# Kernel optimization log

Hardware: AMD Instinct MI355X
Metric: run time of the kernel (lower is better)

## Reference

```python
import jax, jax.numpy as jnp
import numpy as np

B, T, C, H = 4, 4096, 1024, 64  # batch, seq_len, embedding_dimension, head_size


def setup_inputs() -> dict:
    key = jax.random.key(0)
    kx, kq, kk, kv = jax.random.split(key, 4)
    x = jax.random.normal(kx, (B, T, C), dtype=jnp.float32)
    # nn.Linear(C, H, bias=False) -> weight applied as x @ W with W:[C,H]
    s = 1.0 / np.sqrt(C)
    Wq = jax.random.normal(kq, (C, H), dtype=jnp.float32) * s
    Wk = jax.random.normal(kk, (C, H), dtype=jnp.float32) * s
    Wv = jax.random.normal(kv, (C, H), dtype=jnp.float32) * s
    return {"x": x, "Wq": Wq, "Wk": Wk, "Wv": Wv}


def reference(x, Wq, Wk, Wv):
    Bx, Tx, Cx = x.shape
    q = x @ Wq  # [B,T,H]
    k = x @ Wk  # [B,T,H]
    v = x @ Wv  # [B,T,H]
    # NOTE: original scales by C**-0.5 (embedding dim), not head_size**-0.5
    wei = jnp.einsum('bqh,bkh->bqk', q, k) * (Cx ** -0.5)  # [B,T,T]
    causal = jnp.tril(jnp.ones((Tx, Tx), dtype=bool))
    wei = jnp.where(causal, wei, -jnp.inf)
    wei = jax.nn.softmax(wei, axis=-1)
    out = jnp.einsum('bqk,bkh->bqh', wei, v)  # [B,T,H]
    return out
```

## Files before the change

kernel.cpp:

```cpp
#include <hip/hip_runtime.h>
#include <math.h>

#define BATCH 4
#define SEQ   4096
#define EMB   1024
#define HDIM  64
#define NSPLIT 4

typedef __attribute__((ext_vector_type(8))) short bf16x8;
typedef __attribute__((ext_vector_type(4))) float f32x4;
typedef __attribute__((ext_vector_type(16))) float f32x16;
typedef __attribute__((ext_vector_type(4))) unsigned int u32x4;

#define MFMA16(a, b, c) __builtin_amdgcn_mfma_f32_16x16x32_bf16(a, b, c, 0, 0, 0)
#define MFMA32(a, b, c) __builtin_amdgcn_mfma_f32_32x32x16_bf16(a, b, c, 0, 0, 0)
#define ZERO16 (f32x16){0.f,0.f,0.f,0.f,0.f,0.f,0.f,0.f,0.f,0.f,0.f,0.f,0.f,0.f,0.f,0.f}

__device__ __forceinline__ unsigned short f2bf(float f) {
  unsigned int u = __float_as_uint(f);
  u = (u + 0x7FFFu + ((u >> 16) & 1u)) >> 16;
  return (unsigned short)u;
}

__device__ __forceinline__ float fexp2(float x) {
  float r;
  asm("v_exp_f32 %0, %1" : "=v"(r) : "v"(x));
  return r;
}

__global__ __launch_bounds__(256) void wt_kernel(
    const float* __restrict__ Wq, const float* __restrict__ Wk,
    const float* __restrict__ Wv, unsigned short* __restrict__ wt) {
  __shared__ float tile[64][65];
  const int bid = blockIdx.x;
  const int m = bid >> 4, kt = bid & 15;
  const float* W = (m == 0) ? Wq : (m == 1) ? Wk : Wv;
  const int tid = threadIdx.x;
  {
    const int r = tid >> 2, c4 = tid & 3;
    const float* src = W + (size_t)(kt * 64 + r) * 64 + c4 * 16;
#pragma unroll
    for (int j = 0; j < 4; ++j) {
      float4 a = *(const float4*)(src + j * 4);
      tile[r][c4 * 16 + j * 4 + 0] = a.x;
      tile[r][c4 * 16 + j * 4 + 1] = a.y;
      tile[r][c4 * 16 + j * 4 + 2] = a.z;
      tile[r][c4 * 16 + j * 4 + 3] = a.w;
    }
  }
  __syncthreads();
  {
    const int col = tid >> 2, kq = tid & 3;
    unsigned short o[16];
#pragma unroll
    for (int j = 0; j < 16; ++j) o[j] = f2bf(tile[kq * 16 + j][col]);
    unsigned short* dst = wt + (size_t)(m * 64 + col) * 1024 + kt * 64 + kq * 16;
    *(bf16x8*)(dst)     = *(bf16x8*)&o[0];
    *(bf16x8*)(dst + 8) = *(bf16x8*)&o[8];
  }
}

__global__ __launch_bounds__(512) void qkv_mfma_kernel(
    const float* __restrict__ x, const unsigned short* __restrict__ wt,
    unsigned short* __restrict__ qb, unsigned short* __restrict__ kb,
    unsigned short* __restrict__ vt) {
  __shared__ __align__(16) unsigned short xs[64 * 64];
  __shared__ __align__(16) unsigned short ws[192 * 64];
  const int tid  = threadIdx.x;
  const int lane = tid & 63, wid = tid >> 6;
  const int g = lane >> 4, p = lane & 15;
  const int mt = wid >> 2, wq = wid & 3;
  const size_t row0 = (size_t)blockIdx.x * 64;

  const int sr = tid >> 3, sc = tid & 7;
  const float* xp = x + (row0 + sr) * EMB + sc * 8;

  f32x4 acc[2][3];
#pragma unroll
  for (int rt = 0; rt < 2; ++rt)
#pragma unroll
    for (int ct = 0; ct < 3; ++ct) acc[rt][ct] = (f32x4){0.f, 0.f, 0.f, 0.f};

  float4 rx[2];
  bf16x8 rw[3];
#pragma unroll
  for (int j = 0; j < 2; ++j) rx[j] = *(const float4*)(xp + j * 4);
#pragma unroll
  for (int it = 0; it < 3; ++it) {
    int i = tid + it * 512, col = i >> 3, cc = i & 7;
    rw[it] = *(const bf16x8*)(wt + (size_t)col * 1024 + cc * 8);
  }

  for (int kc = 0; kc < 16; ++kc) {
    __syncthreads();
#pragma unroll
    for (int j = 0; j < 2; ++j) {
      ushort4 h;
      h.x = f2bf(rx[j].x); h.y = f2bf(rx[j].y);
      h.z = f2bf(rx[j].z); h.w = f2bf(rx[j].w);
      *(ushort4*)((char*)xs + ((sr * 128 + sc * 16 + j * 8) ^ ((sr & 7) << 4))) = h;
    }
#pragma unroll
    for (int it = 0; it < 3; ++it) {
      int i = tid + it * 512, col = i >> 3, cc = i & 7;
      *(bf16x8*)((char*)ws + ((col * 128 + cc * 16) ^ ((col & 7) << 4))) = rw[it];
    }
    if (kc < 15) {
      const float* xpn = xp + (kc + 1) * 64;
#pragma unroll
      for (int j = 0; j < 2; ++j) rx[j] = *(const float4*)(xpn + j * 4);
#pragma unroll
      for (int it = 0; it < 3; ++it) {
        int i = tid + it * 512, col = i >> 3, cc = i & 7;
        rw[it] = *(const bf16x8*)(wt + (size_t)col * 1024 + (kc + 1) * 64 + cc * 8);
      }
    }
    __syncthreads();
#pragma unroll
    for (int ks = 0; ks < 2; ++ks) {
      bf16x8 af[2];
#pragma unroll
      for (int rt = 0; rt < 2; ++rt) {
        int row = mt * 32 + rt * 16 + p;
        af[rt] = *(const bf16x8*)((char*)xs +
                 ((row * 128 + ks * 64 + g * 16) ^ ((row & 7) << 4)));
      }
#pragma unroll
      for (int ct = 0; ct < 3; ++ct) {
        int col = wq * 48 + ct * 16 + p;
        bf16x8 bfr = *(const bf16x8*)((char*)ws +
                     ((col * 128 + ks * 64 + g * 16) ^ ((col & 7) << 4)));
#pragma unroll
        for (int rt = 0; rt < 2; ++rt)
          acc[rt][ct] = MFMA16(af[rt], bfr, acc[rt][ct]);
      }
    }
  }

  const int b     = (int)(row0 >> 12);
  const int tbase = (int)(row0 & 4095);
  unsigned short* vtb = vt + (((size_t)b * 64 + (tbase >> 6)) * 64) * 64;
#pragma unroll
  for (int rt = 0; rt < 2; ++rt)
#pragma unroll
    for (int ct = 0; ct < 3; ++ct) {
      const int c0  = wq * 48 + ct * 16;
      const int mtx = c0 >> 6;
      const int col = (c0 & 63) + p;
#pragma unroll
      for (int r = 0; r < 4; ++r) {
        const int row = mt * 32 + rt * 16 + 4 * g + r;
        const float vf = acc[rt][ct][r];
        if (mtx == 0)      qb[(row0 + row) * HDIM + col] = f2bf(vf * 0.0450843714f);
        else if (mtx == 1) kb[(row0 + row) * HDIM + col] = f2bf(vf);
        else               vtb[(size_t)col * 64 + row]   = f2bf(vf);
      }
    }
}

__device__ __forceinline__ void tile_body32(
    const unsigned short* __restrict__ sKb, const unsigned short* __restrict__ sVb,
    int qrel, bool diag, const bf16x8 (&qf)[4], int h, int q5,
    float& m, float& l, f32x16& o0, f32x16& o1) {
  const int sw = (q5 & 7) << 4;
  f32x16 s0 = ZERO16, s1 = ZERO16;
#pragma unroll
  for (int st = 0; st < 4; ++st) {
    bf16x8 k0 = *(const bf16x8*)((const char*)sKb + q5 * 128 +
                                 ((32 * st + 16 * h) ^ sw));
    bf16x8 k1 = *(const bf16x8*)((const char*)sKb + (32 + q5) * 128 +
                                 ((32 * st + 16 * h) ^ sw));
    s0 = MFMA32(k0, qf[st], s0);
    s1 = MFMA32(k1, qf[st], s1);
  }
  if (diag) {
#pragma unroll
    for (int r = 0; r < 16; ++r) {
      const int kk = (r & 3) + 8 * (r >> 2) + 4 * h;
      if (kk      > qrel) s0[r] = -1e30f;
      if (kk + 32 > qrel) s1[r] = -1e30f;
    }
  }
  float tm = -3e38f;
#pragma unroll
  for (int r = 0; r < 16; ++r) { tm = fmaxf(tm, s0[r]); tm = fmaxf(tm, s1[r]); }
  tm = fmaxf(tm, __shfl_xor(tm, 32));
  if (__any(tm > m + 11.5f)) {
    float mn = fmaxf(m, tm);
    float c = fexp2(m - mn);
    l *= c; o0 *= c; o1 *= c;
    m = mn;
  }
  float ps = 0.f;
#pragma unroll
  for (int r = 0; r < 16; ++r) {
    float a = fexp2(s0[r] - m); s0[r] = a; ps += a;
    float c2 = fexp2(s1[r] - m); s1[r] = c2; ps += c2;
  }
  ps += __shfl_xor(ps, 32);
  l += ps;
  unsigned W[16];
#pragma unroll
  for (int i = 0; i < 8; ++i) {
    asm("v_cvt_pk_bf16_f32 %0, %1, %2" : "=v"(W[i])     : "v"(s0[2*i]), "v"(s0[2*i+1]));
    asm("v_cvt_pk_bf16_f32 %0, %1, %2" : "=v"(W[8 + i]) : "v"(s1[2*i]), "v"(s1[2*i+1]));
  }
  bf16x8 pf[4];
#pragma unroll
  for (int sG = 0; sG < 4; ++sG) {
    const int ba = 4 * sG;
    unsigned x0 = (unsigned)__shfl_xor((int)W[ba + 0], 32);
    unsigned x1 = (unsigned)__shfl_xor((int)W[ba + 1], 32);
    unsigned x2 = (unsigned)__shfl_xor((int)W[ba + 2], 32);
    unsigned x3 = (unsigned)__shfl_xor((int)W[ba + 3], 32);
    u32x4 fw;
    fw[0] = h ? x2 : W[ba + 0];
    fw[1] = h ? x3 : W[ba + 1];
    fw[2] = h ? W[ba + 2] : x0;
    fw[3] = h ? W[ba + 3] : x1;
    pf[sG] = __builtin_bit_cast(bf16x8, fw);
  }
#pragma unroll
  for (int sG = 0; sG < 4; ++sG) {
    bf16x8 v0 = *(const bf16x8*)((const char*)sVb + q5 * 128 +
                                 ((32 * sG + 16 * h) ^ sw));
    o0 = MFMA32(v0, pf[sG], o0);
    bf16x8 v1 = *(const bf16x8*)((const char*)sVb + (32 + q5) * 128 +
                                 ((32 * sG + 16 * h) ^ sw));
    o1 = MFMA32(v1, pf[sG], o1);
  }
}

__device__ __forceinline__ void item_map128(int g_it, int nA, int nB,
                                            int& kt, bool& isA, bool& diag) {
  if (g_it < nA) { isA = true;  kt = g_it;      diag = (kt >= nA - 2); }
  else           { isA = false; kt = g_it - nA; diag = (kt >= nB - 2); }
}

__global__ __launch_bounds__(512) void attn_partial_kernel(
    const unsigned short* __restrict__ qb, const unsigned short* __restrict__ kbm,
    const unsigned short* __restrict__ vt, float* __restrict__ pw) {
  __shared__ __align__(16) unsigned short sK[2][4096];
  __shared__ __align__(16) unsigned short sV[2][4096];
  const int tid = threadIdx.x;
  const int wid = tid >> 6, lane = tid & 63;
  const int q5 = lane & 31, h = lane >> 5;
  const int bid = blockIdx.x;
  const int sp = bid & 3, j = (bid >> 2) & 15, b = bid >> 6;
  const int jB = 31 - j;
  const int nA = 2 * j + 2, nB = 64 - 2 * j;
  const bool sideA = (wid < 4);
  const int ws = sideA ? wid : wid - 4;
  const int tq0 = sideA ? j * 128 + 32 * ws : jB * 128 + 32 * ws;

  const char* kbase = (const char*)(kbm + (size_t)b * SEQ * HDIM);
  const char* vbase = (const char*)(vt  + (size_t)b * SEQ * HDIM);

  bf16x8 qf[4];
  {
    const unsigned short* qrow = qb + ((size_t)b * SEQ + tq0 + q5) * HDIM;
#pragma unroll
    for (int st = 0; st < 4; ++st)
      qf[st] = *(const bf16x8*)(qrow + 16 * st + 8 * h);
  }

  const int slot = tid * 16;
  const int r0 = slot >> 7, koff = r0 * 128 + ((slot & 127) ^ ((r0 & 7) << 4));

  float m = -1e30f, l = 0.f;
  f32x16 o0 = ZERO16, o1 = ZERO16;

  const int cnt = (66 - sp + NSPLIT - 1) / NSPLIT;

  bf16x8 rk0, rv0;
  {
    int kt; bool isA, diag;
    item_map128(sp, nA, nB, kt, isA, diag);
    rk0 = *(const bf16x8*)(kbase + (size_t)kt * 8192 + koff);
    rv0 = *(const bf16x8*)(vbase + (size_t)kt * 8192 + koff);
  }
  *(bf16x8*)((char*)sK[0] + slot) = rk0;
  *(bf16x8*)((char*)sV[0] + slot) = rv0;
  if (cnt > 1) {
    int kt; bool isA, diag;
    item_map128(sp + NSPLIT, nA, nB, kt, isA, diag);
    rk0 = *(const bf16x8*)(kbase + (size_t)kt * 8192 + koff);
    rv0 = *(const bf16x8*)(vbase + (size_t)kt * 8192 + koff);
  }
  __syncthreads();

  for (int ii = 0; ii < cnt; ++ii) {
    const int buf = ii & 1;
    if (ii + 1 < cnt) {
      const int nb = buf ^ 1;
      *(bf16x8*)((char*)sK[nb] + slot) = rk0;
      *(bf16x8*)((char*)sV[nb] + slot) = rv0;
    }
    if (ii + 2 < cnt) {
      int kt; bool isA, diag;
      item_map128(sp + (ii + 2) * NSPLIT, nA, nB, kt, isA, diag);
      rk0 = *(const bf16x8*)(kbase + (size_t)kt * 8192 + koff);
      rv0 = *(const bf16x8*)(vbase + (size_t)kt * 8192 + koff);
    }
    int kt; bool isA, diag;
    item_map128(sp + ii * NSPLIT, nA, nB, kt, isA, diag);
    if (isA == sideA) {
      tile_body32(sK[buf], sV[buf], tq0 + q5 - kt * 64, diag, qf, h, q5,
                  m, l, o0, o1);
    }
    __syncthreads();
  }

  l += __shfl_xor(l, 32);
  l *= 0.5f;

  const int grp = (sideA ? j * 8 + 2 * ws : jB * 8 + 2 * ws) + (q5 >> 4);
  float* pp = pw + ((size_t)(b * 256 + grp) * NSPLIT + sp) * 1056;
  const int qr = (q5 & 15) * 64;
#pragma unroll
  for (int quad = 0; quad < 4; ++quad) {
    *(f32x4*)(pp + qr + 8 * quad + 4 * h) =
        (f32x4){o0[4 * quad], o0[4 * quad + 1], o0[4 * quad + 2], o0[4 * quad + 3]};
    *(f32x4*)(pp + qr + 32 + 8 * quad + 4 * h) =
        (f32x4){o1[4 * quad], o1[4 * quad + 1], o1[4 * quad + 2], o1[4 * quad + 3]};
  }
  if (h == 0) { pp[1024 + (q5 & 15)] = m; pp[1040 + (q5 & 15)] = l; }
}

__global__ __launch_bounds__(256) void attn_merge_kernel(
    const float* __restrict__ pw, float* __restrict__ out) {
  const int bid = blockIdx.x;
  const int b = bid >> 8, grp = bid & 255;
  const int q = threadIdx.x & 15, db = threadIdx.x >> 4;
  const float* pp = pw + (size_t)bid * NSPLIT * 1056;
  float ms[NSPLIT], ls[NSPLIT];
  float mm = -3e38f;
#pragma unroll
  for (int s = 0; s < NSPLIT; ++s) {
    ms[s] = pp[s * 1056 + 1024 + q];
    ls[s] = pp[s * 1056 + 1040 + q];
    mm = fmaxf(mm, ms[s]);
  }
  float L = 0.f, a0 = 0.f, a1 = 0.f, a2 = 0.f, a3 = 0.f;
#pragma unroll
  for (int s = 0; s < NSPLIT; ++s) {
    float sc = fexp2(ms[s] - mm);
    L += ls[s] * sc;
    float4 v = *(const float4*)(pp + s * 1056 + q * 64 + 4 * db);
    a0 += v.x * sc; a1 += v.y * sc; a2 += v.z * sc; a3 += v.w * sc;
  }
  const float inv = 1.f / L;
  float* op = out + ((size_t)b * SEQ + grp * 16 + q) * HDIM + 4 * db;
  op[0] = a0 * inv; op[1] = a1 * inv; op[2] = a2 * inv; op[3] = a3 * inv;
}

extern "C" void kernel_launch(void* const* d_in, const int* in_sizes, int n_in,
                              void* d_out, int out_size, void* d_ws, size_t ws_size,
                              hipStream_t stream) {
  const float* x  = (const float*)d_in[0];
  const float* Wq = (const float*)d_in[1];
  const float* Wk = (const float*)d_in[2];
  const float* Wv = (const float*)d_in[3];
  float* outp = (float*)d_out;

  const size_t rows = (size_t)BATCH * SEQ;
  unsigned short* qbf = (unsigned short*)d_ws;
  unsigned short* kbf = qbf + rows * HDIM;
  unsigned short* vtb = kbf + rows * HDIM;
  unsigned short* wt  = vtb + rows * HDIM;
  float* pw = (float*)(wt + 192 * 1024);

  wt_kernel<<<dim3(48), dim3(256), 0, stream>>>(Wq, Wk, Wv, wt);
  qkv_mfma_kernel<<<dim3((unsigned)(rows / 64)), dim3(512), 0, stream>>>(x, wt, qbf, kbf, vtb);
  attn_partial_kernel<<<dim3(256), dim3(512), 0, stream>>>(qbf, kbf, vtb, pw);
  attn_merge_kernel<<<dim3(1024), dim3(256), 0, stream>>>(pw, outp);
}
```

Baseline: 56.61 us.

## Process two KV tiles per step with both wave groups handling both query sides

```diff
diff --git a/kernel.cpp b/kernel.cpp
--- a/kernel.cpp
+++ b/kernel.cpp
@@ -240,91 +240,112 @@
 __global__ __launch_bounds__(512) void attn_partial_kernel(
     const unsigned short* __restrict__ qb, const unsigned short* __restrict__ kbm,
     const unsigned short* __restrict__ vt, float* __restrict__ pw) {
-  __shared__ __align__(16) unsigned short sK[2][4096];
-  __shared__ __align__(16) unsigned short sV[2][4096];
+  __shared__ __align__(16) unsigned short sK[4][4096];
+  __shared__ __align__(16) unsigned short sV[4][4096];
   const int tid = threadIdx.x;
   const int wid = tid >> 6, lane = tid & 63;
   const int q5 = lane & 31, h = lane >> 5;
+  const int gg = wid >> 2, ws = wid & 3;
   const int bid = blockIdx.x;
   const int sp = bid & 3, j = (bid >> 2) & 15, b = bid >> 6;
   const int jB = 31 - j;
   const int nA = 2 * j + 2, nB = 64 - 2 * j;
-  const bool sideA = (wid < 4);
-  const int ws = sideA ? wid : wid - 4;
-  const int tq0 = sideA ? j * 128 + 32 * ws : jB * 128 + 32 * ws;
+  const int tq0A = j * 128 + 32 * ws;
+  const int tq0B = jB * 128 + 32 * ws;
 
   const char* kbase = (const char*)(kbm + (size_t)b * SEQ * HDIM);
   const char* vbase = (const char*)(vt  + (size_t)b * SEQ * HDIM);
 
-  bf16x8 qf[4];
-  {
-    const unsigned short* qrow = qb + ((size_t)b * SEQ + tq0 + q5) * HDIM;
-#pragma unroll
-    for (int st = 0; st < 4; ++st)
-      qf[st] = *(const bf16x8*)(qrow + 16 * st + 8 * h);
+  bf16x8 qfA[4], qfB[4];
+  {
+    const unsigned short* qra = qb + ((size_t)b * SEQ + tq0A + q5) * HDIM;
+    const unsigned short* qrb = qb + ((size_t)b * SEQ + tq0B + q5) * HDIM;
+#pragma unroll
+    for (int st = 0; st < 4; ++st) {
+      qfA[st] = *(const bf16x8*)(qra + 16 * st + 8 * h);
+      qfB[st] = *(const bf16x8*)(qrb + 16 * st + 8 * h);
+    }
   }
 
   const int slot = tid * 16;
   const int r0 = slot >> 7, koff = r0 * 128 + ((slot & 127) ^ ((r0 & 7) << 4));
 
-  float m = -1e30f, l = 0.f;
-  f32x16 o0 = ZERO16, o1 = ZERO16;
+  float mA = -1e30f, lA = 0.f, mB = -1e30f, lB = 0.f;
+  f32x16 oA0 = ZERO16, oA1 = ZERO16, oB0 = ZERO16, oB1 = ZERO16;
 
   const int cnt = (66 - sp + NSPLIT - 1) / NSPLIT;
 
-  bf16x8 rk0, rv0;
-  {
-    int kt; bool isA, diag;
-    item_map128(sp, nA, nB, kt, isA, diag);
-    rk0 = *(const bf16x8*)(kbase + (size_t)kt * 8192 + koff);
-    rv0 = *(const bf16x8*)(vbase + (size_t)kt * 8192 + koff);
-  }
-  *(bf16x8*)((char*)sK[0] + slot) = rk0;
-  *(bf16x8*)((char*)sV[0] + slot) = rv0;
-  if (cnt > 1) {
-    int kt; bool isA, diag;
-    item_map128(sp + NSPLIT, nA, nB, kt, isA, diag);
-    rk0 = *(const bf16x8*)(kbase + (size_t)kt * 8192 + koff);
-    rv0 = *(const bf16x8*)(vbase + (size_t)kt * 8192 + koff);
-  }
+#define LOAD_ITEM(t, rk, rv) do {                                        \
+    int kt_; bool isA_, diag_;                                           \
+    item_map128(sp + (t) * NSPLIT, nA, nB, kt_, isA_, diag_);            \
+    rk = *(const bf16x8*)(kbase + (size_t)kt_ * 8192 + koff);            \
+    rv = *(const bf16x8*)(vbase + (size_t)kt_ * 8192 + koff);            \
+  } while (0)
+
+#define WRITE_BUF(bi, rk, rv) do {                                       \
+    *(bf16x8*)((char*)sK[bi] + slot) = rk;                               \
+    *(bf16x8*)((char*)sV[bi] + slot) = rv;                               \
+  } while (0)
+
+  bf16x8 rkE, rvE, rkO, rvO;
+  LOAD_ITEM(0, rkE, rvE);
+  WRITE_BUF(0, rkE, rvE);
+  if (1 < cnt) { LOAD_ITEM(1, rkO, rvO); WRITE_BUF(1, rkO, rvO); }
+  if (2 < cnt) LOAD_ITEM(2, rkE, rvE);
+  if (3 < cnt) LOAD_ITEM(3, rkO, rvO);
   __syncthreads();
 
-  for (int ii = 0; ii < cnt; ++ii) {
-    const int buf = ii & 1;
-    if (ii + 1 < cnt) {
-      const int nb = buf ^ 1;
-      *(bf16x8*)((char*)sK[nb] + slot) = rk0;
-      *(bf16x8*)((char*)sV[nb] + slot) = rv0;
-    }
-    if (ii + 2 < cnt) {
+  const int npr = (cnt + 1) >> 1;
+  for (int pr = 0; pr < npr; ++pr) {
+    const int pb = pr & 1, nb = pb ^ 1;
+    const int t0 = 2 * pr, t1 = 2 * pr + 1;
+    if (t0 + 2 < cnt) WRITE_BUF(nb * 2 + 0, rkE, rvE);
+    if (t1 + 2 < cnt) WRITE_BUF(nb * 2 + 1, rkO, rvO);
+    if (t0 + 4 < cnt) LOAD_ITEM(t0 + 4, rkE, rvE);
+    if (t1 + 4 < cnt) LOAD_ITEM(t1 + 4, rkO, rvO);
+    const int t = 2 * pr + gg;
+    if (t < cnt) {
       int kt; bool isA, diag;
-      item_map128(sp + (ii + 2) * NSPLIT, nA, nB, kt, isA, diag);
-      rk0 = *(const bf16x8*)(kbase + (size_t)kt * 8192 + koff);
-      rv0 = *(const bf16x8*)(vbase + (size_t)kt * 8192 + koff);
-    }
-    int kt; bool isA, diag;
-    item_map128(sp + ii * NSPLIT, nA, nB, kt, isA, diag);
-    if (isA == sideA) {
-      tile_body32(sK[buf], sV[buf], tq0 + q5 - kt * 64, diag, qf, h, q5,
-                  m, l, o0, o1);
+      item_map128(sp + t * NSPLIT, nA, nB, kt, isA, diag);
+      const int bi = pb * 2 + gg;
+      if (isA) tile_body32(sK[bi], sV[bi], tq0A + q5 - kt * 64, diag, qfA,
+                           h, q5, mA, lA, oA0, oA1);
+      else     tile_body32(sK[bi], sV[bi], tq0B + q5 - kt * 64, diag, qfB,
+                           h, q5, mB, lB, oB0, oB1);
     }
     __syncthreads();
   }
 
-  l += __shfl_xor(l, 32);
-  l *= 0.5f;
-
-  const int grp = (sideA ? j * 8 + 2 * ws : jB * 8 + 2 * ws) + (q5 >> 4);
-  float* pp = pw + ((size_t)(b * 256 + grp) * NSPLIT + sp) * 1056;
-  const int qr = (q5 & 15) * 64;
-#pragma unroll
-  for (int quad = 0; quad < 4; ++quad) {
-    *(f32x4*)(pp + qr + 8 * quad + 4 * h) =
-        (f32x4){o0[4 * quad], o0[4 * quad + 1], o0[4 * quad + 2], o0[4 * quad + 3]};
-    *(f32x4*)(pp + qr + 32 + 8 * quad + 4 * h) =
-        (f32x4){o1[4 * quad], o1[4 * quad + 1], o1[4 * quad + 2], o1[4 * quad + 3]};
-  }
-  if (h == 0) { pp[1024 + (q5 & 15)] = m; pp[1040 + (q5 & 15)] = l; }
+#undef LOAD_ITEM
+#undef WRITE_BUF
+
+  const int s8 = gg * NSPLIT + sp;
+  {
+    const int grpA = j * 8 + 2 * ws + (q5 >> 4);
+    float* pp = pw + ((size_t)(b * 256 + grpA) * (NSPLIT * 2) + s8) * 1056;
+    const int qr = (q5 & 15) * 64;
+#pragma unroll
+    for (int quad = 0; quad < 4; ++quad) {
+      *(f32x4*)(pp + qr + 8 * quad + 4 * h) =
+          (f32x4){oA0[4 * quad], oA0[4 * quad + 1], oA0[4 * quad + 2], oA0[4 * quad + 3]};
+      *(f32x4*)(pp + qr + 32 + 8 * quad + 4 * h) =
+          (f32x4){oA1[4 * quad], oA1[4 * quad + 1], oA1[4 * quad + 2], oA1[4 * quad + 3]};
+    }
+    if (h == 0) { pp[1024 + (q5 & 15)] = mA; pp[1040 + (q5 & 15)] = lA; }
+  }
+  {
+    const int grpB = jB * 8 + 2 * ws + (q5 >> 4);
+    float* pp = pw + ((size_t)(b * 256 + grpB) * (NSPLIT * 2) + s8) * 1056;
+    const int qr = (q5 & 15) * 64;
+#pragma unroll
+    for (int quad = 0; quad < 4; ++quad) {
+      *(f32x4*)(pp + qr + 8 * quad + 4 * h) =
+          (f32x4){oB0[4 * quad], oB0[4 * quad + 1], oB0[4 * quad + 2], oB0[4 * quad + 3]};
+      *(f32x4*)(pp + qr + 32 + 8 * quad + 4 * h) =
+          (f32x4){oB1[4 * quad], oB1[4 * quad + 1], oB1[4 * quad + 2], oB1[4 * quad + 3]};
+    }
+    if (h == 0) { pp[1024 + (q5 & 15)] = mB; pp[1040 + (q5 & 15)] = lB; }
+  }
 }
 
 __global__ __launch_bounds__(256) void attn_merge_kernel(
@@ -332,18 +353,18 @@
   const int bid = blockIdx.x;
   const int b = bid >> 8, grp = bid & 255;
   const int q = threadIdx.x & 15, db = threadIdx.x >> 4;
-  const float* pp = pw + (size_t)bid * NSPLIT * 1056;
-  float ms[NSPLIT], ls[NSPLIT];
+  const float* pp = pw + (size_t)bid * (NSPLIT * 2) * 1056;
+  float ms[NSPLIT * 2], ls[NSPLIT * 2];
   float mm = -3e38f;
 #pragma unroll
-  for (int s = 0; s < NSPLIT; ++s) {
+  for (int s = 0; s < NSPLIT * 2; ++s) {
     ms[s] = pp[s * 1056 + 1024 + q];
     ls[s] = pp[s * 1056 + 1040 + q];
     mm = fmaxf(mm, ms[s]);
   }
   float L = 0.f, a0 = 0.f, a1 = 0.f, a2 = 0.f, a3 = 0.f;
 #pragma unroll
-  for (int s = 0; s < NSPLIT; ++s) {
+  for (int s = 0; s < NSPLIT * 2; ++s) {
     float sc = fexp2(ms[s] - mm);
     L += ls[s] * sc;
     float4 v = *(const float4*)(pp + s * 1056 + q * 64 + 4 * db);
```

After: 58.68 us. 3.7% more time.
